# Performance work log

Hardware: AMD Instinct MI355X
Metric: run time of the kernel (lower is better)

The kernel has to match this reference:

```python
import jax, jax.numpy as jnp
import numpy as np

TEMPERATURE = 0.07


def setup_inputs() -> dict:
    key = jax.random.key(0)
    k1, k2 = jax.random.split(key)
    B, V, C, H, W = 4, 2, 128, 32, 32
    features = jax.random.normal(k1, (B, V, C, H, W), dtype=jnp.float32)
    # L2-normalize per-pixel feature vectors (channel dim), as contrastive
    # embeddings are in practice; the original exp() is unstabilized.
    features = features / jnp.linalg.norm(features, axis=2, keepdims=True)
    labels = jax.random.randint(k2, (B, V, H, W), 0, 4, dtype=jnp.int32)
    return {"features": features, "labels": labels}


def reference(features, labels):
    B, V, C, H, W = features.shape
    # torch.cat(torch.unbind(features, dim=1), dim=0): views stacked along batch
    cf = jnp.transpose(features, (1, 0, 2, 3, 4)).reshape(B * V, C, H, W)
    # kernels = cf.permute(0,2,3,1).reshape(-1, C, 1, 1); conv2d with 1x1 kernels
    # == pairwise dot products of per-pixel feature vectors.
    X = jnp.transpose(cf, (0, 2, 3, 1)).reshape(-1, C)  # [N, C], N = B*V*H*W
    N = X.shape[0]
    logits = (X @ X.T) / TEMPERATURE  # [N, N]

    lab = jnp.transpose(labels, (1, 0, 2, 3)).reshape(-1)  # [N]
    mask = (lab[:, None] == lab[None, :]).astype(logits.dtype)  # [N, N]
    logits_mask = 1.0 - jnp.eye(N, dtype=logits.dtype)  # zero the diagonal
    mask = mask * logits_mask

    exp_logits = jnp.exp(logits) * logits_mask
    log_prob = logits - jnp.log(jnp.sum(exp_logits, axis=1, keepdims=True))
    mean_log_prob_pos = jnp.sum(mask * log_prob, axis=1) / jnp.sum(mask, axis=1)
    loss = -mean_log_prob_pos  # [N]

    non_bg = (lab != 0).astype(logits.dtype)
    return jnp.sum(loss * non_bg) / jnp.sum(non_bg)
```

## Files before the change

kernel.cpp:

```cpp
#include <hip/hip_runtime.h>
#include <hip/hip_bf16.h>
#include <stdint.h>

typedef short bf16x8 __attribute__((ext_vector_type(8)));
typedef float f32x16 __attribute__((ext_vector_type(16)));

#define NROWS 8192
#define CDIM  128
#define TEMP  0.07f
#define C1F   20.6099291555566248f

__device__ __forceinline__ float bf2f(unsigned short u) {
  union { unsigned int i; float f; } x; x.i = ((unsigned int)u) << 16; return x.f;
}
__device__ __forceinline__ unsigned short f2bf(float f) {
  union { float f; unsigned int i; } x; x.f = f;
  unsigned int r = x.i + 0x7fffu + ((x.i >> 16) & 1u);
  return (unsigned short)(r >> 16);
}
__device__ __forceinline__ float fexp2(float x) {
#if __has_builtin(__builtin_amdgcn_exp2f)
  return __builtin_amdgcn_exp2f(x);
#else
  return exp2f(x);
#endif
}

__global__ __launch_bounds__(256) void k_pack(const float* __restrict__ F,
                                              unsigned short* __restrict__ Xb) {
  __shared__ float lds[128 * 33];
  const int g   = blockIdx.x >> 5;
  const int hw0 = (blockIdx.x & 31) << 5;
  const int tid = threadIdx.x;
#pragma unroll
  for (int p = 0; p < 16; ++p) {
    int c  = p * 8 + (tid >> 5);
    int hw = hw0 + (tid & 31);
    lds[c * 33 + (tid & 31)] = F[(g * 128 + c) * 1024 + hw];
  }
  __syncthreads();
#pragma unroll
  for (int p = 0; p < 16; ++p) {
    int hwl = p * 2 + (tid >> 7);
    int c   = tid & 127;
    int row = g * 1024 + hw0 + hwl;
    Xb[row * 128 + c] = f2bf(lds[c * 33 + hwl]);
  }
}

__global__ __launch_bounds__(256) void k_gsum(const unsigned short* __restrict__ Xb,
                                              const int* __restrict__ labels,
                                              float* __restrict__ G,
                                              int* __restrict__ hist) {
  const int tid    = threadIdx.x;
  const int lane   = tid & 63;
  const int rchunk = blockIdx.x >> 3;
  const int cbase  = (blockIdx.x & 7) * 16;
  const int cl     = tid & 15;
  const int rg     = tid >> 4;
  float a0 = 0.f, a1 = 0.f, a2 = 0.f, a3 = 0.f;
  const int nend = rchunk * 512 + 512;
  for (int n = rchunk * 512 + rg; n < nend; n += 16) {
    int   lab = labels[n];
    float v   = bf2f(Xb[n * 128 + cbase + cl]);
    a0 += (lab == 0) ? v : 0.f;
    a1 += (lab == 1) ? v : 0.f;
    a2 += (lab == 2) ? v : 0.f;
    a3 += (lab == 3) ? v : 0.f;
  }
  a0 += __shfl_xor(a0, 16, 64); a0 += __shfl_xor(a0, 32, 64);
  a1 += __shfl_xor(a1, 16, 64); a1 += __shfl_xor(a1, 32, 64);
  a2 += __shfl_xor(a2, 16, 64); a2 += __shfl_xor(a2, 32, 64);
  a3 += __shfl_xor(a3, 16, 64); a3 += __shfl_xor(a3, 32, 64);
  if (lane < 16) {
    int c = cbase + lane;
    atomicAdd(&G[0 * 128 + c], a0);
    atomicAdd(&G[1 * 128 + c], a1);
    atomicAdd(&G[2 * 128 + c], a2);
    atomicAdd(&G[3 * 128 + c], a3);
  }
  if (blockIdx.x == 0) {
    int h0 = 0, h1 = 0, h2 = 0, h3 = 0;
    for (int n = tid; n < NROWS; n += 256) {
      int lab = labels[n];
      h0 += (lab == 0); h1 += (lab == 1); h2 += (lab == 2); h3 += (lab == 3);
    }
    for (int m = 1; m < 64; m <<= 1) {
      h0 += __shfl_xor(h0, m, 64); h1 += __shfl_xor(h1, m, 64);
      h2 += __shfl_xor(h2, m, 64); h3 += __shfl_xor(h3, m, 64);
    }
    if (lane == 0) {
      atomicAdd(&hist[0], h0); atomicAdd(&hist[1], h1);
      atomicAdd(&hist[2], h2); atomicAdd(&hist[3], h3);
    }
  }
}

__global__ __launch_bounds__(256, 4) void k_main(const unsigned short* __restrict__ Xb,
                                                 float* __restrict__ S) {
  __shared__ int4 ldsB[2][16 * 33];
  const int tid      = threadIdx.x;
  const int lane     = tid & 63;
  const int wave     = tid >> 6;
  const int rowBlock = blockIdx.x >> 4;
  const int split    = blockIdx.x & 15;
  const int r0       = rowBlock * 128 + wave * 32;
  const int col0     = split * 512;
  const int m        = lane & 31;
  const int half     = lane >> 5;

  bf16x8 afrag[8];
#pragma unroll
  for (int s = 0; s < 8; ++s)
    afrag[s] = *(const bf16x8*)(Xb + (r0 + m) * CDIM + (half + 2 * s) * 8);

  float accS[16];
#pragma unroll
  for (int r = 0; r < 16; ++r) accS[r] = 0.f;

  const int n_l = tid >> 3;
  const int bq  = tid & 7;
  const unsigned short* src = Xb + (col0 + n_l) * CDIM + bq * 16;
  int4 v0 = *(const int4*)src;
  int4 v1 = *(const int4*)(src + 8);
  ldsB[0][(2 * bq) * 33 + n_l]     = v0;
  ldsB[0][(2 * bq + 1) * 33 + n_l] = v1;
  src += 32 * CDIM;
  v0 = *(const int4*)src;
  v1 = *(const int4*)(src + 8);

  for (int t = 0; t < 16; ++t) {
    __syncthreads();
    if (t < 15) {
      ldsB[(t + 1) & 1][(2 * bq) * 33 + n_l]     = v0;
      ldsB[(t + 1) & 1][(2 * bq + 1) * 33 + n_l] = v1;
    }
    if (t < 14) {
      src += 32 * CDIM;
      v0 = *(const int4*)src;
      v1 = *(const int4*)(src + 8);
    }
    const int cur = t & 1;
    f32x16 acc;
#pragma unroll
    for (int r = 0; r < 16; ++r) acc[r] = 0.f;
#pragma unroll
    for (int s = 0; s < 8; ++s) {
      bf16x8 bfrag = *(const bf16x8*)&ldsB[cur][(half + 2 * s) * 33 + m];
      acc = __builtin_amdgcn_mfma_f32_32x32x16_bf16(afrag[s], bfrag, acc, 0, 0, 0);
    }
    const int colbase = col0 + t * 32;
    if (r0 == colbase) {
      const int colg = colbase + m;
#pragma unroll
      for (int r = 0; r < 16; ++r) {
        int   row = r0 + (r & 3) + 8 * (r >> 2) + 4 * half;
        float arg = (row == colg) ? -1e30f : acc[r] * C1F;
        accS[r] += fexp2(arg);
      }
    } else {
#pragma unroll
      for (int r = 0; r < 16; ++r) accS[r] += fexp2(acc[r] * C1F);
    }
  }

#pragma unroll
  for (int r = 0; r < 16; ++r) {
    float v = accS[r];
    v += __shfl_xor(v, 1, 64);
    v += __shfl_xor(v, 2, 64);
    v += __shfl_xor(v, 4, 64);
    v += __shfl_xor(v, 8, 64);
    v += __shfl_xor(v, 16, 64);
    accS[r] = v;
  }
  if (m == 0) {
#pragma unroll
    for (int r = 0; r < 16; ++r) {
      int row = r0 + (r & 3) + 8 * (r >> 2) + 4 * half;
      atomicAdd(&S[row], accS[r]);
    }
  }
}

__global__ __launch_bounds__(256) void k_loss(const unsigned short* __restrict__ Xb,
                                              const int* __restrict__ labels,
                                              const float* __restrict__ S,
                                              const float* __restrict__ G,
                                              const int* __restrict__ hist,
                                              float* __restrict__ sumLoss) {
  const int i   = blockIdx.x * 256 + threadIdx.x;
  const int lab = labels[i];
  const float* g = G + lab * 128;
  const unsigned short* x = Xb + i * CDIM;
  float dot = 0.f, nrm = 0.f;
#pragma unroll
  for (int cc = 0; cc < 16; ++cc) {
    int4 q = *(const int4*)(x + cc * 8);
    const unsigned int* qs = (const unsigned int*)&q;
#pragma unroll
    for (int j = 0; j < 4; ++j) {
      unsigned int u = qs[j];
      float lo = __uint_as_float(u << 16);
      float hi = __uint_as_float(u & 0xffff0000u);
      int   ci = cc * 8 + j * 2;
      dot += lo * g[ci] + hi * g[ci + 1];
      nrm += lo * lo + hi * hi;
    }
  }
  float Si   = S[i];
  float cnt  = (float)(hist[lab] - 1);
  float loss = logf(Si) - (dot - nrm) / (TEMP * cnt);
  float contrib = (lab != 0) ? loss : 0.f;
  for (int mm = 1; mm < 64; mm <<= 1) contrib += __shfl_xor(contrib, mm, 64);
  __shared__ float ws4[4];
  if ((threadIdx.x & 63) == 0) ws4[threadIdx.x >> 6] = contrib;
  __syncthreads();
  if (threadIdx.x == 0) atomicAdd(sumLoss, ws4[0] + ws4[1] + ws4[2] + ws4[3]);
}

__global__ void k_final(const float* __restrict__ sumLoss,
                        const int* __restrict__ hist,
                        float* __restrict__ out) {
  out[0] = sumLoss[0] / (float)(NROWS - hist[0]);
}

extern "C" void kernel_launch(void* const* d_in, const int* in_sizes, int n_in,
                              void* d_out, int out_size, void* d_ws, size_t ws_size,
                              hipStream_t stream) {
  const float* F      = (const float*)d_in[0];
  const int*   labels = (const int*)d_in[1];
  char* ws = (char*)d_ws;

  unsigned short* Xb      = (unsigned short*)ws;
  const size_t    offS    = (size_t)NROWS * CDIM * 2;
  float*          S       = (float*)(ws + offS);
  float*          G       = (float*)(ws + offS + 32768);
  int*            hist    = (int*)(ws + offS + 32768 + 2048);
  float*          sumLoss = (float*)(ws + offS + 32768 + 2048 + 16);

  hipMemsetAsync(ws + offS, 0, 32768 + 2048 + 16 + 4, stream);

  hipLaunchKernelGGL(k_pack, dim3(256), dim3(256), 0, stream, F, Xb);
  hipLaunchKernelGGL(k_gsum, dim3(128), dim3(256), 0, stream, Xb, labels, G, hist);
  hipLaunchKernelGGL(k_main, dim3(1024), dim3(256), 0, stream, Xb, S);
  hipLaunchKernelGGL(k_loss, dim3(32), dim3(256), 0, stream, Xb, labels, S, G, hist, sumLoss);
  hipLaunchKernelGGL(k_final, dim3(1), dim3(1), 0, stream, sumLoss, hist, (float*)d_out);
}
```

Before: 110.2 us.

## Fuse label sums into pack, drop memset and final kernel, register-tile main GEMM

The per-label channel sums and histogram move into the pack kernel as per-block partials. These are reduced by extra blocks appended to the main kernel, and the workspace zeroing is done inside pack, so the memset and the separate gsum kernel go away. The final division is folded into the loss kernel through a last-block ticket. The main kernel now has each wave compute two 32-row tiles and load B fragments straight from global memory into double-buffered registers instead of through LDS with barriers. Occupancy drops to two blocks, and the gather reads of B are uncoalesced.

```diff
diff --git a/kernel.cpp b/kernel.cpp
--- a/kernel.cpp
+++ b/kernel.cpp
@@ -9,6 +9,15 @@
 #define CDIM  128
 #define TEMP  0.07f
 #define C1F   20.6099291555566248f
+
+#define OFF_S     2097152
+#define OFF_SUM   2129920
+#define OFF_TKT   2129924
+#define OFF_G     2129984
+#define OFF_HIST  2132032
+#define OFF_GPART 2132096
+#define OFF_HPART 2656384
+#define ZWORDS    8194
 
 __device__ __forceinline__ float bf2f(unsigned short u) {
   union { unsigned int i; float f; } x; x.i = ((unsigned int)u) << 16; return x.f;
@@ -27,11 +36,30 @@
 }
 
 __global__ __launch_bounds__(256) void k_pack(const float* __restrict__ F,
-                                              unsigned short* __restrict__ Xb) {
+                                              const int* __restrict__ labels,
+                                              char* __restrict__ ws) {
+  unsigned short* Xb    = (unsigned short*)ws;
+  float*          zbase = (float*)(ws + OFF_S);
+  float*          Gpart = (float*)(ws + OFF_GPART);
+  int*            Hpart = (int*)(ws + OFF_HPART);
+
   __shared__ float lds[128 * 33];
-  const int g   = blockIdx.x >> 5;
-  const int hw0 = (blockIdx.x & 31) << 5;
+  __shared__ float gp[2][4][128];
+  __shared__ int   lab_lds[32];
+
   const int tid = threadIdx.x;
+  const int bid = blockIdx.x;
+
+  {
+    int idx = bid * 256 + tid;
+    if (idx < ZWORDS) zbase[idx] = 0.0f;
+  }
+
+  const int g   = bid >> 5;
+  const int hw0 = (bid & 31) << 5;
+  const int n0  = g * 1024 + hw0;
+  if (tid < 32) lab_lds[tid] = labels[n0 + tid];
+
 #pragma unroll
   for (int p = 0; p < 16; ++p) {
     int c  = p * 8 + (tid >> 5);
@@ -39,159 +67,171 @@
     lds[c * 33 + (tid & 31)] = F[(g * 128 + c) * 1024 + hw];
   }
   __syncthreads();
+
+  const int c = tid & 127;
+  const int h = tid >> 7;
+  float a0 = 0.f, a1 = 0.f, a2 = 0.f, a3 = 0.f;
 #pragma unroll
   for (int p = 0; p < 16; ++p) {
-    int hwl = p * 2 + (tid >> 7);
-    int c   = tid & 127;
-    int row = g * 1024 + hw0 + hwl;
-    Xb[row * 128 + c] = f2bf(lds[c * 33 + hwl]);
-  }
-}
-
-__global__ __launch_bounds__(256) void k_gsum(const unsigned short* __restrict__ Xb,
-                                              const int* __restrict__ labels,
-                                              float* __restrict__ G,
-                                              int* __restrict__ hist) {
-  const int tid    = threadIdx.x;
-  const int lane   = tid & 63;
-  const int rchunk = blockIdx.x >> 3;
-  const int cbase  = (blockIdx.x & 7) * 16;
-  const int cl     = tid & 15;
-  const int rg     = tid >> 4;
-  float a0 = 0.f, a1 = 0.f, a2 = 0.f, a3 = 0.f;
-  const int nend = rchunk * 512 + 512;
-  for (int n = rchunk * 512 + rg; n < nend; n += 16) {
-    int   lab = labels[n];
-    float v   = bf2f(Xb[n * 128 + cbase + cl]);
+    int hwl = p * 2 + h;
+    float vf = lds[c * 33 + hwl];
+    unsigned short vb = f2bf(vf);
+    Xb[(n0 + hwl) * 128 + c] = vb;
+    float v  = bf2f(vb);
+    int  lab = lab_lds[hwl];
     a0 += (lab == 0) ? v : 0.f;
     a1 += (lab == 1) ? v : 0.f;
     a2 += (lab == 2) ? v : 0.f;
     a3 += (lab == 3) ? v : 0.f;
   }
-  a0 += __shfl_xor(a0, 16, 64); a0 += __shfl_xor(a0, 32, 64);
-  a1 += __shfl_xor(a1, 16, 64); a1 += __shfl_xor(a1, 32, 64);
-  a2 += __shfl_xor(a2, 16, 64); a2 += __shfl_xor(a2, 32, 64);
-  a3 += __shfl_xor(a3, 16, 64); a3 += __shfl_xor(a3, 32, 64);
-  if (lane < 16) {
-    int c = cbase + lane;
-    atomicAdd(&G[0 * 128 + c], a0);
-    atomicAdd(&G[1 * 128 + c], a1);
-    atomicAdd(&G[2 * 128 + c], a2);
-    atomicAdd(&G[3 * 128 + c], a3);
-  }
-  if (blockIdx.x == 0) {
-    int h0 = 0, h1 = 0, h2 = 0, h3 = 0;
-    for (int n = tid; n < NROWS; n += 256) {
-      int lab = labels[n];
-      h0 += (lab == 0); h1 += (lab == 1); h2 += (lab == 2); h3 += (lab == 3);
-    }
-    for (int m = 1; m < 64; m <<= 1) {
-      h0 += __shfl_xor(h0, m, 64); h1 += __shfl_xor(h1, m, 64);
-      h2 += __shfl_xor(h2, m, 64); h3 += __shfl_xor(h3, m, 64);
-    }
-    if (lane == 0) {
-      atomicAdd(&hist[0], h0); atomicAdd(&hist[1], h1);
-      atomicAdd(&hist[2], h2); atomicAdd(&hist[3], h3);
-    }
-  }
-}
-
-__global__ __launch_bounds__(256, 4) void k_main(const unsigned short* __restrict__ Xb,
-                                                 float* __restrict__ S) {
-  __shared__ int4 ldsB[2][16 * 33];
-  const int tid      = threadIdx.x;
-  const int lane     = tid & 63;
-  const int wave     = tid >> 6;
-  const int rowBlock = blockIdx.x >> 4;
-  const int split    = blockIdx.x & 15;
-  const int r0       = rowBlock * 128 + wave * 32;
-  const int col0     = split * 512;
-  const int m        = lane & 31;
-  const int half     = lane >> 5;
-
-  bf16x8 afrag[8];
-#pragma unroll
-  for (int s = 0; s < 8; ++s)
-    afrag[s] = *(const bf16x8*)(Xb + (r0 + m) * CDIM + (half + 2 * s) * 8);
-
-  float accS[16];
-#pragma unroll
-  for (int r = 0; r < 16; ++r) accS[r] = 0.f;
-
-  const int n_l = tid >> 3;
-  const int bq  = tid & 7;
-  const unsigned short* src = Xb + (col0 + n_l) * CDIM + bq * 16;
-  int4 v0 = *(const int4*)src;
-  int4 v1 = *(const int4*)(src + 8);
-  ldsB[0][(2 * bq) * 33 + n_l]     = v0;
-  ldsB[0][(2 * bq + 1) * 33 + n_l] = v1;
-  src += 32 * CDIM;
-  v0 = *(const int4*)src;
-  v1 = *(const int4*)(src + 8);
-
-  for (int t = 0; t < 16; ++t) {
-    __syncthreads();
-    if (t < 15) {
-      ldsB[(t + 1) & 1][(2 * bq) * 33 + n_l]     = v0;
-      ldsB[(t + 1) & 1][(2 * bq + 1) * 33 + n_l] = v1;
-    }
-    if (t < 14) {
-      src += 32 * CDIM;
-      v0 = *(const int4*)src;
-      v1 = *(const int4*)(src + 8);
-    }
-    const int cur = t & 1;
-    f32x16 acc;
-#pragma unroll
-    for (int r = 0; r < 16; ++r) acc[r] = 0.f;
-#pragma unroll
-    for (int s = 0; s < 8; ++s) {
-      bf16x8 bfrag = *(const bf16x8*)&ldsB[cur][(half + 2 * s) * 33 + m];
-      acc = __builtin_amdgcn_mfma_f32_32x32x16_bf16(afrag[s], bfrag, acc, 0, 0, 0);
-    }
-    const int colbase = col0 + t * 32;
+  gp[h][0][c] = a0; gp[h][1][c] = a1; gp[h][2][c] = a2; gp[h][3][c] = a3;
+  __syncthreads();
+  if (tid < 128) {
+#pragma unroll
+    for (int l = 0; l < 4; ++l)
+      Gpart[bid * 512 + l * 128 + tid] = gp[0][l][tid] + gp[1][l][tid];
+  }
+  if (tid < 4) {
+    int hh = 0;
+#pragma unroll
+    for (int r = 0; r < 32; ++r) hh += (lab_lds[r] == tid);
+    Hpart[bid * 4 + tid] = hh;
+  }
+}
+
+__global__ __launch_bounds__(256, 2) void k_main(const unsigned short* __restrict__ Xb,
+                                                 char* __restrict__ ws) {
+  float* S     = (float*)(ws + OFF_S);
+  float* Gpart = (float*)(ws + OFF_GPART);
+  int*   Hpart = (int*)(ws + OFF_HPART);
+  float* G     = (float*)(ws + OFF_G);
+  int*   hist  = (int*)(ws + OFF_HIST);
+
+  const int bid = blockIdx.x;
+  const int tid = threadIdx.x;
+
+  if (bid >= 512) {
+    const int rb2 = bid - 512;
+    const int e   = rb2 * 128 + (tid >> 1);
+    const int hh  = tid & 1;
+    float s = 0.f;
+    for (int b = hh * 128; b < hh * 128 + 128; ++b) s += Gpart[b * 512 + e];
+    s += __shfl_xor(s, 1, 64);
+    if (hh == 0) G[e] = s;
+    if (rb2 == 0 && tid < 4) {
+      int cth = 0;
+      for (int b = 0; b < 256; ++b) cth += Hpart[b * 4 + tid];
+      hist[tid] = cth;
+    }
+    return;
+  }
+
+  const int lane = tid & 63;
+  const int wave = tid >> 6;
+  const int m    = lane & 31;
+  const int half = lane >> 5;
+  const int rb   = bid >> 4;
+  const int sp   = bid & 15;
+  const int r0   = rb * 256 + wave * 64;
+  const int col0 = sp * 512;
+
+  bf16x8 afrag[2][8];
+#pragma unroll
+  for (int rs = 0; rs < 2; ++rs)
+#pragma unroll
+    for (int s = 0; s < 8; ++s)
+      afrag[rs][s] = *(const bf16x8*)(Xb + (r0 + rs * 32 + m) * CDIM + half * 8 + s * 16);
+
+  float accS0[16], accS1[16];
+#pragma unroll
+  for (int r = 0; r < 16; ++r) { accS0[r] = 0.f; accS1[r] = 0.f; }
+
+  const unsigned short* bptr = Xb + (col0 + m) * CDIM + half * 8;
+  bf16x8 bf[2][8];
+#pragma unroll
+  for (int s = 0; s < 8; ++s) bf[0][s] = *(const bf16x8*)(bptr + s * 16);
+
+#pragma unroll 2
+  for (int g = 0; g < 16; ++g) {
+    const int p = g & 1;
+    if (g < 15) {
+      const unsigned short* np = bptr + (g + 1) * 32 * CDIM;
+#pragma unroll
+      for (int s = 0; s < 8; ++s) bf[p ^ 1][s] = *(const bf16x8*)(np + s * 16);
+    }
+    f32x16 a0, a1;
+#pragma unroll
+    for (int r = 0; r < 16; ++r) { a0[r] = 0.f; a1[r] = 0.f; }
+#pragma unroll
+    for (int s = 0; s < 8; ++s)
+      a0 = __builtin_amdgcn_mfma_f32_32x32x16_bf16(afrag[0][s], bf[p][s], a0, 0, 0, 0);
+#pragma unroll
+    for (int s = 0; s < 8; ++s)
+      a1 = __builtin_amdgcn_mfma_f32_32x32x16_bf16(afrag[1][s], bf[p][s], a1, 0, 0, 0);
+
+    const int colbase = col0 + g * 32;
     if (r0 == colbase) {
       const int colg = colbase + m;
 #pragma unroll
       for (int r = 0; r < 16; ++r) {
         int   row = r0 + (r & 3) + 8 * (r >> 2) + 4 * half;
-        float arg = (row == colg) ? -1e30f : acc[r] * C1F;
-        accS[r] += fexp2(arg);
+        float arg = (row == colg) ? -1e30f : a0[r] * C1F;
+        accS0[r] += fexp2(arg);
       }
     } else {
 #pragma unroll
-      for (int r = 0; r < 16; ++r) accS[r] += fexp2(acc[r] * C1F);
+      for (int r = 0; r < 16; ++r) accS0[r] += fexp2(a0[r] * C1F);
+    }
+    if (r0 + 32 == colbase) {
+      const int colg = colbase + m;
+#pragma unroll
+      for (int r = 0; r < 16; ++r) {
+        int   row = r0 + 32 + (r & 3) + 8 * (r >> 2) + 4 * half;
+        float arg = (row == colg) ? -1e30f : a1[r] * C1F;
+        accS1[r] += fexp2(arg);
+      }
+    } else {
+#pragma unroll
+      for (int r = 0; r < 16; ++r) accS1[r] += fexp2(a1[r] * C1F);
     }
   }
 
 #pragma unroll
   for (int r = 0; r < 16; ++r) {
-    float v = accS[r];
-    v += __shfl_xor(v, 1, 64);
-    v += __shfl_xor(v, 2, 64);
-    v += __shfl_xor(v, 4, 64);
-    v += __shfl_xor(v, 8, 64);
+    float v = accS0[r];
+    v += __shfl_xor(v, 1, 64);  v += __shfl_xor(v, 2, 64);
+    v += __shfl_xor(v, 4, 64);  v += __shfl_xor(v, 8, 64);
     v += __shfl_xor(v, 16, 64);
-    accS[r] = v;
+    accS0[r] = v;
+    float w = accS1[r];
+    w += __shfl_xor(w, 1, 64);  w += __shfl_xor(w, 2, 64);
+    w += __shfl_xor(w, 4, 64);  w += __shfl_xor(w, 8, 64);
+    w += __shfl_xor(w, 16, 64);
+    accS1[r] = w;
   }
   if (m == 0) {
 #pragma unroll
     for (int r = 0; r < 16; ++r) {
-      int row = r0 + (r & 3) + 8 * (r >> 2) + 4 * half;
-      atomicAdd(&S[row], accS[r]);
+      int rr = (r & 3) + 8 * (r >> 2) + 4 * half;
+      atomicAdd(&S[r0 + rr], accS0[r]);
+      atomicAdd(&S[r0 + 32 + rr], accS1[r]);
     }
   }
 }
 
 __global__ __launch_bounds__(256) void k_loss(const unsigned short* __restrict__ Xb,
                                               const int* __restrict__ labels,
-                                              const float* __restrict__ S,
-                                              const float* __restrict__ G,
-                                              const int* __restrict__ hist,
-                                              float* __restrict__ sumLoss) {
+                                              char* __restrict__ ws,
+                                              float* __restrict__ out) {
+  const float* S       = (const float*)(ws + OFF_S);
+  const float* G       = (const float*)(ws + OFF_G);
+  const int*   hist    = (const int*)(ws + OFF_HIST);
+  float*       sumLoss = (float*)(ws + OFF_SUM);
+  int*         ticket  = (int*)(ws + OFF_TKT);
+
   const int i   = blockIdx.x * 256 + threadIdx.x;
   const int lab = labels[i];
-  const float* g = G + lab * 128;
+  const float* gl = G + lab * 128;
   const unsigned short* x = Xb + i * CDIM;
   float dot = 0.f, nrm = 0.f;
 #pragma unroll
@@ -204,7 +244,7 @@
       float lo = __uint_as_float(u << 16);
       float hi = __uint_as_float(u & 0xffff0000u);
       int   ci = cc * 8 + j * 2;
-      dot += lo * g[ci] + hi * g[ci + 1];
+      dot += lo * gl[ci] + hi * gl[ci + 1];
       nrm += lo * lo + hi * hi;
     }
   }
@@ -216,13 +256,15 @@
   __shared__ float ws4[4];
   if ((threadIdx.x & 63) == 0) ws4[threadIdx.x >> 6] = contrib;
   __syncthreads();
-  if (threadIdx.x == 0) atomicAdd(sumLoss, ws4[0] + ws4[1] + ws4[2] + ws4[3]);
-}
-
-__global__ void k_final(const float* __restrict__ sumLoss,
-                        const int* __restrict__ hist,
-                        float* __restrict__ out) {
-  out[0] = sumLoss[0] / (float)(NROWS - hist[0]);
+  if (threadIdx.x == 0) {
+    atomicAdd(sumLoss, ws4[0] + ws4[1] + ws4[2] + ws4[3]);
+    __threadfence();
+    int t = atomicAdd(ticket, 1);
+    if (t == 31) {
+      float total = atomicAdd(sumLoss, 0.0f);
+      out[0] = total / (float)(NROWS - hist[0]);
+    }
+  }
 }
 
 extern "C" void kernel_launch(void* const* d_in, const int* in_sizes, int n_in,
@@ -231,19 +273,10 @@
   const float* F      = (const float*)d_in[0];
   const int*   labels = (const int*)d_in[1];
   char* ws = (char*)d_ws;
-
-  unsigned short* Xb      = (unsigned short*)ws;
-  const size_t    offS    = (size_t)NROWS * CDIM * 2;
-  float*          S       = (float*)(ws + offS);
-  float*          G       = (float*)(ws + offS + 32768);
-  int*            hist    = (int*)(ws + offS + 32768 + 2048);
-  float*          sumLoss = (float*)(ws + offS + 32768 + 2048 + 16);
-
-  hipMemsetAsync(ws + offS, 0, 32768 + 2048 + 16 + 4, stream);
-
-  hipLaunchKernelGGL(k_pack, dim3(256), dim3(256), 0, stream, F, Xb);
-  hipLaunchKernelGGL(k_gsum, dim3(128), dim3(256), 0, stream, Xb, labels, G, hist);
-  hipLaunchKernelGGL(k_main, dim3(1024), dim3(256), 0, stream, Xb, S);
-  hipLaunchKernelGGL(k_loss, dim3(32), dim3(256), 0, stream, Xb, labels, S, G, hist, sumLoss);
-  hipLaunchKernelGGL(k_final, dim3(1), dim3(1), 0, stream, sumLoss, hist, (float*)d_out);
-}
+  unsigned short* Xb = (unsigned short*)ws;
+
+  hipLaunchKernelGGL(k_pack, dim3(256), dim3(256), 0, stream, F, labels, ws);
+  hipLaunchKernelGGL(k_main, dim3(516), dim3(256), 0, stream, Xb, ws);
+  hipLaunchKernelGGL(k_loss, dim3(32), dim3(256), 0, stream, Xb, labels, ws,
+                     (float*)d_out);
+}
```

Measured after the change: 113.4 us. 2.9% more time.
